# Performance work log

Hardware: AMD Instinct MI355X
Metric: run time of the kernel (lower is better)

The kernel has to match this reference:

```python
import jax, jax.numpy as jnp
import numpy as np

B, L, D = 2, 2048, 2048
HQ, HKV = 32, 8
HD = D // HQ            # 64
G = HQ // HKV           # 4


def setup_inputs() -> dict:
    key = jax.random.key(0)
    ks = jax.random.split(key, 9)
    s = 1.0 / np.sqrt(D)
    return {
        "x": jax.random.normal(ks[0], (B, L, D), jnp.float32),
        "Wq": jax.random.normal(ks[1], (D, HQ * HD), jnp.float32) * s,
        "bq": jnp.zeros((HQ * HD,), jnp.float32),
        "Wk": jax.random.normal(ks[2], (D, HKV * HD), jnp.float32) * s,
        "bk": jnp.zeros((HKV * HD,), jnp.float32),
        "Wv": jax.random.normal(ks[3], (D, HKV * HD), jnp.float32) * s,
        "bv": jnp.zeros((HKV * HD,), jnp.float32),
        "Wo": jax.random.normal(ks[4], (HQ * HD, D), jnp.float32) * s,
        "bo": jnp.zeros((D,), jnp.float32),
    }


def reference(x, Wq, bq, Wk, bk, Wv, bv, Wo, bo):
    # projections
    q = x @ Wq + bq                                   # [B, L, HQ*HD]
    k = x @ Wk + bk                                   # [B, L, HKV*HD]
    v = x @ Wv + bv
    # split heads; group q heads by kv head: [B, HKV, G, L, HD]
    q = q.reshape(B, L, HKV, G, HD).transpose(0, 2, 3, 1, 4)
    k = k.reshape(B, L, HKV, HD).transpose(0, 2, 1, 3)   # [B, HKV, L, HD]
    v = v.reshape(B, L, HKV, HD).transpose(0, 2, 1, 3)
    scale = 1.0 / np.sqrt(HD)
    # scores [B, HKV, G, Lq, Lk] -- same math as repeat_kv + matmul
    scores = jnp.einsum('bhgqd,bhkd->bhgqk', q, k) * scale
    attn = jax.nn.softmax(scores, axis=-1)
    ctx = jnp.einsum('bhgqk,bhkd->bhgqd', attn, v)       # [B, HKV, G, L, HD]
    # merge heads back to [B, L, HQ*HD]
    ctx = ctx.transpose(0, 3, 1, 2, 4).reshape(B, L, HQ * HD)
    return ctx @ Wo + bo
```

## Files before the change

kernel.cpp:

```cpp
#include <hip/hip_runtime.h>
#include <cstdint>
#include <cstring>


#define L_SEQ 2048
#define D_MODEL 2048
#define M_ROWS 4096
#define KV_COLS 512
#define ATTN_SCALE 0.18033688011112042f

typedef __bf16 bf16x8 __attribute__((ext_vector_type(8)));
typedef float f32x4 __attribute__((ext_vector_type(4)));
typedef float f32x16 __attribute__((ext_vector_type(16)));

__device__ __forceinline__ f32x4 zero4() {
    f32x4 v; v[0] = 0.f; v[1] = 0.f; v[2] = 0.f; v[3] = 0.f; return v;
}

__device__ __forceinline__ unsigned short f2bf(float x) {
    unsigned u = __builtin_bit_cast(unsigned, x);
    u = (u + 0x7FFFu + ((u >> 16) & 1u)) >> 16;
    return (unsigned short)u;
}

__device__ __forceinline__ unsigned pk_bf16(float a, float b) {
#if __has_builtin(__builtin_amdgcn_cvt_pk_bf16_f32)
    typedef __bf16 bf16x2 __attribute__((ext_vector_type(2)));
    bf16x2 r = __builtin_amdgcn_cvt_pk_bf16_f32(a, b);
    return __builtin_bit_cast(unsigned, r);
#else
    return (unsigned)f2bf(a) | ((unsigned)f2bf(b) << 16);
#endif
}

__device__ __forceinline__ f32x4 mfma16(uint4 a, uint4 b, f32x4 c) {
    return __builtin_amdgcn_mfma_f32_16x16x32_bf16(
        __builtin_bit_cast(bf16x8, a), __builtin_bit_cast(bf16x8, b), c, 0, 0, 0);
}
__device__ __forceinline__ f32x16 mfma32(uint4 a, uint4 b, f32x16 c) {
    return __builtin_amdgcn_mfma_f32_32x32x16_bf16(
        __builtin_bit_cast(bf16x8, a), __builtin_bit_cast(bf16x8, b), c, 0, 0, 0);
}

__device__ __forceinline__ void gl_lds16(const unsigned short* g, unsigned short* l) {
    __builtin_amdgcn_global_load_lds(
        (const __attribute__((address_space(1))) unsigned int*)g,
        (__attribute__((address_space(3))) unsigned int*)l, 16, 0, 0);
}

#if __has_builtin(__builtin_amdgcn_exp2f)
#define EXP2F(x) __builtin_amdgcn_exp2f(x)
#else
#define EXP2F(x) exp2f(x)
#endif

__device__ __forceinline__ void permswap32(unsigned& a, unsigned& b) {
    asm("v_permlane32_swap_b32 %0, %1" : "+v"(a), "+v"(b));
}


__global__ __launch_bounds__(256) void cast_x_kernel(const float* __restrict__ in,
                                                     unsigned short* __restrict__ out,
                                                     int n4) {
    int i = blockIdx.x * 256 + threadIdx.x;
    if (i >= n4) return;
    float4 v = ((const float4*)in)[i];
    uint2 o;
    o.x = pk_bf16(v.x, v.y);
    o.y = pk_bf16(v.z, v.w);
    ((uint2*)out)[i] = o;
}

__global__ __launch_bounds__(256) void transpose_cast_kernel(const float* __restrict__ in,
                                                             unsigned short* __restrict__ out,
                                                             int N, int row_off) {
    __shared__ float tile[32][33];
    const int n0 = blockIdx.x * 32, k0 = blockIdx.y * 32;
    const int tc = threadIdx.x & 31, tr = threadIdx.x >> 5;
#pragma unroll
    for (int i = 0; i < 4; ++i)
        tile[tr + i * 8][tc] = in[(size_t)(k0 + tr + i * 8) * N + n0 + tc];
    __syncthreads();
#pragma unroll
    for (int i = 0; i < 4; ++i)
        out[(size_t)(row_off + n0 + tr + i * 8) * 2048 + k0 + tc] = f2bf(tile[tc][tr + i * 8]);
}

__global__ __launch_bounds__(256) void transpose_v_kernel(const unsigned short* __restrict__ Vb,
                                                          unsigned short* __restrict__ Vt) {
    __shared__ unsigned short tile[32][33];
    const int c0 = blockIdx.x * 32, l0 = blockIdx.y * 32, b = blockIdx.z;
    const int tc = threadIdx.x & 31, tr = threadIdx.x >> 5;
#pragma unroll
    for (int i = 0; i < 4; ++i)
        tile[tr + i * 8][tc] = Vb[(size_t)(b * 2048 + l0 + tr + i * 8) * KV_COLS + c0 + tc];
    __syncthreads();
#pragma unroll
    for (int i = 0; i < 4; ++i)
        Vt[(size_t)(b * 512 + c0 + tr + i * 8) * 2048 + l0 + tc] = tile[tc][tr + i * 8];
}


__device__ __forceinline__ void gemm_core_2048(const unsigned short* __restrict__ A,
                                               const unsigned short* __restrict__ Bt,
                                               int m_block, int n_block,
                                               unsigned short* smA, unsigned short* smB,
                                               f32x4 acc[4][4]) {
    const int tid = threadIdx.x;
    const int w = tid >> 6, lane = tid & 63;
    const int wm = w >> 1, wn = w & 1;
    const int lr = lane & 15, lg = lane >> 4;

#pragma unroll
    for (int i = 0; i < 4; ++i)
#pragma unroll
        for (int j = 0; j < 4; ++j) acc[i][j] = zero4();

    const int rowA = m_block * 128 + w * 32 + (lane >> 2);
    const int rowB = n_block * 128 + w * 32 + (lane >> 2);
    const int kcol = (lane & 3) * 8;
    const unsigned short* gA0 = A + (size_t)rowA * 2048 + kcol;
    const unsigned short* gA1 = gA0 + (size_t)16 * 2048;
    const unsigned short* gB0 = Bt + (size_t)rowB * 2048 + kcol;
    const unsigned short* gB1 = gB0 + (size_t)16 * 2048;
    unsigned short* lA0 = smA + (w * 32) * 32;
    unsigned short* lA1 = smA + (w * 32 + 16) * 32;
    unsigned short* lB0 = smB + (w * 32) * 32;
    unsigned short* lB1 = smB + (w * 32 + 16) * 32;

    for (int kt = 0; kt < 64; ++kt) {
        gl_lds16(gA0 + kt * 32, lA0);
        gl_lds16(gA1 + kt * 32, lA1);
        gl_lds16(gB0 + kt * 32, lB0);
        gl_lds16(gB1 + kt * 32, lB1);
        __syncthreads();
        uint4 af[4], bfg[4];
#pragma unroll
        for (int i = 0; i < 4; ++i)
            af[i] = *(const uint4*)(smA + (wm * 64 + i * 16 + lr) * 32 + lg * 8);
#pragma unroll
        for (int j = 0; j < 4; ++j)
            bfg[j] = *(const uint4*)(smB + (wn * 64 + j * 16 + lr) * 32 + lg * 8);
#pragma unroll
        for (int i = 0; i < 4; ++i)
#pragma unroll
            for (int j = 0; j < 4; ++j)
                acc[i][j] = mfma16(af[i], bfg[j], acc[i][j]);
        __syncthreads();
    }
}

__global__ __launch_bounds__(256) void gemm_qkv_kernel(
    const unsigned short* __restrict__ Xb, const unsigned short* __restrict__ Wt,
    const float* __restrict__ bq, const float* __restrict__ bk, const float* __restrict__ bv,
    unsigned short* __restrict__ Qb, unsigned short* __restrict__ Kb,
    unsigned short* __restrict__ Vb) {
    __shared__ __align__(16) unsigned short smA[128 * 32];
    __shared__ __align__(16) unsigned short smB[128 * 32];
    f32x4 acc[4][4];
    gemm_core_2048(Xb, Wt, blockIdx.x, blockIdx.y, smA, smB, acc);

    const int tid = threadIdx.x;
    const int w = tid >> 6, lane = tid & 63;
    const int wm = w >> 1, wn = w & 1;
    const int lr = lane & 15, lg = lane >> 4;
    const int nbase = blockIdx.y * 128;

    unsigned short* outp; int ldo, noff; const float* bias; float scale;
    if (nbase < 2048)      { outp = Qb; ldo = 2048; noff = 0;    bias = bq; scale = 1.f; }
    else if (nbase < 2560) { outp = Kb; ldo = 512;  noff = 2048; bias = bk; scale = ATTN_SCALE; }
    else                   { outp = Vb; ldo = 512;  noff = 2560; bias = bv; scale = 1.f; }

#pragma unroll
    for (int i = 0; i < 4; ++i) {
        const int mrow = blockIdx.x * 128 + wm * 64 + i * 16 + lg * 4;
#pragma unroll
        for (int j = 0; j < 4; ++j) {
            const int nloc = nbase + wn * 64 + j * 16 + lr - noff;
            const float bb = bias[nloc];
#pragma unroll
            for (int r = 0; r < 4; ++r)
                outp[(size_t)(mrow + r) * ldo + nloc] = f2bf((acc[i][j][r] + bb) * scale);
        }
    }
}

__global__ __launch_bounds__(256) void gemm_out_kernel(
    const unsigned short* __restrict__ Cb, const unsigned short* __restrict__ Wot,
    const float* __restrict__ bo, float* __restrict__ out) {
    __shared__ __align__(16) unsigned short smA[128 * 32];
    __shared__ __align__(16) unsigned short smB[128 * 32];
    f32x4 acc[4][4];
    gemm_core_2048(Cb, Wot, blockIdx.x, blockIdx.y, smA, smB, acc);

    const int tid = threadIdx.x;
    const int w = tid >> 6, lane = tid & 63;
    const int wm = w >> 1, wn = w & 1;
    const int lr = lane & 15, lg = lane >> 4;

#pragma unroll
    for (int i = 0; i < 4; ++i) {
        const int mrow = blockIdx.x * 128 + wm * 64 + i * 16 + lg * 4;
#pragma unroll
        for (int j = 0; j < 4; ++j) {
            const int ncol = blockIdx.y * 128 + wn * 64 + j * 16 + lr;
            const float bb = bo[ncol];
#pragma unroll
            for (int r = 0; r < 4; ++r)
                out[(size_t)(mrow + r) * 2048 + ncol] = acc[i][j][r] + bb;
        }
    }
}


__global__ __launch_bounds__(512, 2) void attn_kernel(const unsigned short* __restrict__ Qb,
                                                      const unsigned short* __restrict__ Kb,
                                                      const unsigned short* __restrict__ Vtg,
                                                      unsigned short* __restrict__ ctx) {
    __shared__ __align__(16) unsigned short smem[32768];

    const int qt = blockIdx.x, hq = blockIdx.y, b = blockIdx.z;
    const int kvh = hq >> 2;
    const int tid = threadIdx.x;
    const int w = tid >> 6, lane = tid & 63;
    const int l31 = lane & 31, h = lane >> 5;

    const int qbase = qt * 512 + w * 64;
    uint4 qf[2][4];
#pragma unroll
    for (int u = 0; u < 2; ++u) {
        const unsigned short* qp =
            Qb + (size_t)(b * L_SEQ + qbase + u * 32 + l31) * 2048 + hq * 64;
#pragma unroll
        for (int dh = 0; dh < 4; ++dh)
            qf[u][dh] = *(const uint4*)(qp + dh * 16 + h * 8);
    }

    f32x16 o00, o01, o10, o11;
#pragma unroll
    for (int r = 0; r < 16; ++r) { o00[r] = 0.f; o01[r] = 0.f; o10[r] = 0.f; o11[r] = 0.f; }
    float l_acc0 = 0.f, l_acc1 = 0.f;

    const size_t kbase = (size_t)(b * L_SEQ) * KV_COLS + kvh * 64;
    const size_t vbase = (size_t)((b * 8 + kvh) * 64) * 2048;

    const int rrk = lane >> 3, cpk = lane & 7;
    const int drv = lane >> 4, cpv = lane & 15;

    unsigned short* ksC = smem;
    unsigned short* vtC = smem + 8192;
    unsigned short* ksN = smem + 16384;
    unsigned short* vtN = smem + 24576;

    auto stage = [&](int T, unsigned short* KS, unsigned short* VT) {
        const int k0s = T * 128;
#pragma unroll
        for (int s = 0; s < 2; ++s) {
            const int blk = w * 2 + s;
            gl_lds16(Kb + kbase + (size_t)(k0s + blk * 8 + rrk) * KV_COLS + ((cpk ^ rrk) * 8),
                     KS + blk * 512);
            const int d = blk * 4 + drv;
            gl_lds16(Vtg + vbase + (size_t)d * 2048 + k0s + ((cpv ^ (d & 15)) * 8),
                     VT + blk * 512);
        }
    };

    stage(0, ksC, vtC);
    __syncthreads();

    for (int t = 0; t < 16; ++t) {
        if (t < 15) stage(t + 1, ksN, vtN);

#pragma unroll
        for (int c = 0; c < 4; ++c) {
            uint4 kf[4];
#pragma unroll
            for (int dh = 0; dh < 4; ++dh)
                kf[dh] = *(const uint4*)&ksC[(c * 32 + l31) * 64 +
                                             (((dh * 2 + h) ^ (l31 & 7)) * 8)];
            unsigned E0[4][2], E1[4][2];
#pragma unroll
            for (int u = 0; u < 2; ++u) {
                f32x16 s;
#pragma unroll
                for (int r = 0; r < 16; ++r) s[r] = 0.f;
                __builtin_amdgcn_s_setprio(1);
#pragma unroll
                for (int dh = 0; dh < 4; ++dh) s = mfma32(kf[dh], qf[u][dh], s);
                __builtin_amdgcn_s_setprio(0);
                float lsum = 0.f;
#pragma unroll
                for (int g = 0; g < 4; ++g) {
                    float e0 = EXP2F(s[4 * g + 0]);
                    float e1 = EXP2F(s[4 * g + 1]);
                    float e2 = EXP2F(s[4 * g + 2]);
                    float e3 = EXP2F(s[4 * g + 3]);
                    lsum += (e0 + e1) + (e2 + e3);
                    if (u == 0) { E0[g][0] = pk_bf16(e0, e1); E0[g][1] = pk_bf16(e2, e3); }
                    else        { E1[g][0] = pk_bf16(e0, e1); E1[g][1] = pk_bf16(e2, e3); }
                }
                if (u == 0) l_acc0 += lsum; else l_acc1 += lsum;
            }
#pragma unroll
            for (int tau = 0; tau < 2; ++tau) {
                const int pos = ((c * 4 + tau * 2 + h) ^ (l31 & 15)) * 8;
                uint4 vf0 = *(const uint4*)&vtC[(size_t)l31 * 128 + pos];
                uint4 vf1 = *(const uint4*)&vtC[(size_t)(32 + l31) * 128 + pos];
                {
                    unsigned x0 = E0[2 * tau][0], z0 = E0[2 * tau + 1][0];
                    unsigned x1 = E0[2 * tau][1], z1 = E0[2 * tau + 1][1];
                    permswap32(x0, z0);
                    permswap32(x1, z1);
                    uint4 pf; pf.x = x0; pf.y = x1; pf.z = z0; pf.w = z1;
                    __builtin_amdgcn_s_setprio(1);
                    o00 = mfma32(vf0, pf, o00);
                    o01 = mfma32(vf1, pf, o01);
                    __builtin_amdgcn_s_setprio(0);
                }
                {
                    unsigned x0 = E1[2 * tau][0], z0 = E1[2 * tau + 1][0];
                    unsigned x1 = E1[2 * tau][1], z1 = E1[2 * tau + 1][1];
                    permswap32(x0, z0);
                    permswap32(x1, z1);
                    uint4 pf; pf.x = x0; pf.y = x1; pf.z = z0; pf.w = z1;
                    __builtin_amdgcn_s_setprio(1);
                    o10 = mfma32(vf0, pf, o10);
                    o11 = mfma32(vf1, pf, o11);
                    __builtin_amdgcn_s_setprio(0);
                }
            }
        }

        __syncthreads();
        unsigned short* tk = ksC; ksC = ksN; ksN = tk;
        unsigned short* tv = vtC; vtC = vtN; vtN = tv;
    }

    unsigned* ep = (unsigned*)smem + w * 1088;
#pragma unroll
    for (int u = 0; u < 2; ++u) {
        const float la = u ? l_acc1 : l_acc0;
        const float l_tot = la + __shfl_xor(la, 32, 64);
        const float rl = 1.f / l_tot;
#pragma unroll
        for (int dt = 0; dt < 2; ++dt) {
            const f32x16& o = u ? (dt ? o11 : o10) : (dt ? o01 : o00);
#pragma unroll
            for (int g = 0; g < 4; ++g)
#pragma unroll
                for (int p = 0; p < 2; ++p) {
                    const int dv = dt * 16 + 4 * g + 2 * h + p;
                    ep[l31 * 34 + dv] =
                        pk_bf16(o[4 * g + 2 * p] * rl, o[4 * g + 2 * p + 1] * rl);
                }
        }
        __builtin_amdgcn_s_waitcnt(0);
#pragma unroll
        for (int p = 0; p < 4; ++p) {
            const int qr = (lane >> 3) + p * 8;
            const int cch = lane & 7;
            uint4 vv = *(const uint4*)((const unsigned short*)ep + qr * 68 + cch * 8);
            *(uint4*)(ctx + (size_t)(b * L_SEQ + qbase + u * 32 + qr) * 2048 +
                      hq * 64 + cch * 8) = vv;
        }
        __builtin_amdgcn_s_waitcnt(0);
    }
}


extern "C" void kernel_launch(void* const* d_in, const int* in_sizes, int n_in,
                              void* d_out, int out_size, void* d_ws, size_t ws_size,
                              hipStream_t stream) {
    const float* x  = (const float*)d_in[0];
    const float* Wq = (const float*)d_in[1];
    const float* bq = (const float*)d_in[2];
    const float* Wk = (const float*)d_in[3];
    const float* bk = (const float*)d_in[4];
    const float* Wv = (const float*)d_in[5];
    const float* bv = (const float*)d_in[6];
    const float* Wo = (const float*)d_in[7];
    const float* bo = (const float*)d_in[8];
    float* out = (float*)d_out;

    char* ws = (char*)d_ws;
    size_t off = 0;
    auto alloc = [&](size_t bytes) {
        char* p = ws + off;
        off += (bytes + 255) & ~(size_t)255;
        return p;
    };
    unsigned short* Wqkvt = (unsigned short*)alloc((size_t)3072 * 2048 * 2);
    unsigned short* Wot   = (unsigned short*)alloc((size_t)2048 * 2048 * 2);
    unsigned short* Xb    = (unsigned short*)alloc((size_t)M_ROWS * 2048 * 2);
    unsigned short* Qb    = (unsigned short*)alloc((size_t)M_ROWS * 2048 * 2);
    unsigned short* Kb    = (unsigned short*)alloc((size_t)M_ROWS * KV_COLS * 2);
    unsigned short* Vb    = (unsigned short*)alloc((size_t)M_ROWS * KV_COLS * 2);
    unsigned short* Vt    = (unsigned short*)alloc((size_t)M_ROWS * KV_COLS * 2);
    unsigned short* Cb    = Xb;

    cast_x_kernel<<<(M_ROWS * 2048 / 4 + 255) / 256, 256, 0, stream>>>(x, Xb,
                                                                       M_ROWS * 2048 / 4);
    transpose_cast_kernel<<<dim3(64, 64), 256, 0, stream>>>(Wq, Wqkvt, 2048, 0);
    transpose_cast_kernel<<<dim3(16, 64), 256, 0, stream>>>(Wk, Wqkvt, 512, 2048);
    transpose_cast_kernel<<<dim3(16, 64), 256, 0, stream>>>(Wv, Wqkvt, 512, 2560);
    transpose_cast_kernel<<<dim3(64, 64), 256, 0, stream>>>(Wo, Wot, 2048, 0);
    gemm_qkv_kernel<<<dim3(32, 24), 256, 0, stream>>>(Xb, Wqkvt, bq, bk, bv, Qb, Kb, Vb);
    transpose_v_kernel<<<dim3(16, 64, 2), 256, 0, stream>>>(Vb, Vt);
    attn_kernel<<<dim3(4, 32, 2), 512, 0, stream>>>(Qb, Kb, Vt, Cb);
    gemm_out_kernel<<<dim3(32, 16), 256, 0, stream>>>(Cb, Wot, bo, out);
}
```

Before: 319.0 us.

## Triple-buffer attention K/V tiles with vmcnt barriers and remap blocks to XCDs

The attention kernel now keeps three LDS buffers instead of two and prefetches K/V tiles two iterations ahead. Per-iteration __syncthreads is replaced by an s_waitcnt vmcnt(N) plus s_barrier, so later loads can stay in flight. The 3D grid becomes a 1D grid of 256 blocks with a swizzle that places the four query tiles of a head (same KV) on the same XCD for L2 reuse. LDS use per block grows from 64KB to 96KB, which may cut occupancy below the two blocks per CU requested by the launch bounds.

```diff
diff --git a/kernel.cpp b/kernel.cpp
--- a/kernel.cpp
+++ b/kernel.cpp
@@ -56,6 +56,19 @@
 
 __device__ __forceinline__ void permswap32(unsigned& a, unsigned& b) {
     asm("v_permlane32_swap_b32 %0, %1" : "+v"(a), "+v"(b));
+}
+
+__device__ __forceinline__ void bar_vm(int keep ) {
+}
+__device__ __forceinline__ void bar_vm4() {
+    asm volatile("s_waitcnt vmcnt(4)" ::: "memory");
+    __builtin_amdgcn_s_barrier();
+    asm volatile("" ::: "memory");
+}
+__device__ __forceinline__ void bar_vm0() {
+    asm volatile("s_waitcnt vmcnt(0)" ::: "memory");
+    __builtin_amdgcn_s_barrier();
+    asm volatile("" ::: "memory");
 }
 
 
@@ -217,10 +230,15 @@
                                                       const unsigned short* __restrict__ Kb,
                                                       const unsigned short* __restrict__ Vtg,
                                                       unsigned short* __restrict__ ctx) {
-    __shared__ __align__(16) unsigned short smem[32768];
-
-    const int qt = blockIdx.x, hq = blockIdx.y, b = blockIdx.z;
+    __shared__ __align__(16) unsigned short smem[49152];
+
+    const int p = blockIdx.x;
+    const int x = p & 7, j = p >> 3;
+    const int group = x * 8 + (j >> 2);
+    const int qt = j & 3;
+    const int hq = group & 31, b = group >> 5;
     const int kvh = hq >> 2;
+
     const int tid = threadIdx.x;
     const int w = tid >> 6, lane = tid & 63;
     const int l31 = lane & 31, h = lane >> 5;
@@ -247,12 +265,13 @@
     const int rrk = lane >> 3, cpk = lane & 7;
     const int drv = lane >> 4, cpv = lane & 15;
 
-    unsigned short* ksC = smem;
-    unsigned short* vtC = smem + 8192;
-    unsigned short* ksN = smem + 16384;
-    unsigned short* vtN = smem + 24576;
-
-    auto stage = [&](int T, unsigned short* KS, unsigned short* VT) {
+    unsigned short* bC  = smem;
+    unsigned short* bN  = smem + 16384;
+    unsigned short* bNN = smem + 32768;
+
+    auto stage = [&](int T, unsigned short* SL) {
+        unsigned short* KS = SL;
+        unsigned short* VT = SL + 8192;
         const int k0s = T * 128;
 #pragma unroll
         for (int s = 0; s < 2; ++s) {
@@ -265,11 +284,15 @@
         }
     };
 
-    stage(0, ksC, vtC);
-    __syncthreads();
+    stage(0, bC);
+    stage(1, bN);
+    bar_vm4();
 
     for (int t = 0; t < 16; ++t) {
-        if (t < 15) stage(t + 1, ksN, vtN);
+        if (t <= 13) stage(t + 2, bNN);
+
+        unsigned short* ksC = bC;
+        unsigned short* vtC = bC + 8192;
 
 #pragma unroll
         for (int c = 0; c < 4; ++c) {
@@ -331,11 +354,14 @@
             }
         }
 
-        __syncthreads();
-        unsigned short* tk = ksC; ksC = ksN; ksN = tk;
-        unsigned short* tv = vtC; vtC = vtN; vtN = tv;
-    }
-
+        if (t <= 13)      bar_vm4();
+        else if (t == 14) bar_vm0();
+        else              { __builtin_amdgcn_s_barrier(); asm volatile("" ::: "memory"); }
+
+        unsigned short* tmp = bC; bC = bN; bN = bNN; bNN = tmp;
+    }
+
+    __syncthreads();
     unsigned* ep = (unsigned*)smem + w * 1088;
 #pragma unroll
     for (int u = 0; u < 2; ++u) {
@@ -348,16 +374,16 @@
 #pragma unroll
             for (int g = 0; g < 4; ++g)
 #pragma unroll
-                for (int p = 0; p < 2; ++p) {
-                    const int dv = dt * 16 + 4 * g + 2 * h + p;
+                for (int pq = 0; pq < 2; ++pq) {
+                    const int dv = dt * 16 + 4 * g + 2 * h + pq;
                     ep[l31 * 34 + dv] =
-                        pk_bf16(o[4 * g + 2 * p] * rl, o[4 * g + 2 * p + 1] * rl);
+                        pk_bf16(o[4 * g + 2 * pq] * rl, o[4 * g + 2 * pq + 1] * rl);
                 }
         }
         __builtin_amdgcn_s_waitcnt(0);
 #pragma unroll
-        for (int p = 0; p < 4; ++p) {
-            const int qr = (lane >> 3) + p * 8;
+        for (int pq = 0; pq < 4; ++pq) {
+            const int qr = (lane >> 3) + pq * 8;
             const int cch = lane & 7;
             uint4 vv = *(const uint4*)((const unsigned short*)ep + qr * 68 + cch * 8);
             *(uint4*)(ctx + (size_t)(b * L_SEQ + qbase + u * 32 + qr) * 2048 +
@@ -406,6 +432,6 @@
     transpose_cast_kernel<<<dim3(64, 64), 256, 0, stream>>>(Wo, Wot, 2048, 0);
     gemm_qkv_kernel<<<dim3(32, 24), 256, 0, stream>>>(Xb, Wqkvt, bq, bk, bv, Qb, Kb, Vb);
     transpose_v_kernel<<<dim3(16, 64, 2), 256, 0, stream>>>(Vb, Vt);
-    attn_kernel<<<dim3(4, 32, 2), 512, 0, stream>>>(Qb, Kb, Vt, Cb);
+    attn_kernel<<<dim3(256), 512, 0, stream>>>(Qb, Kb, Vt, Cb);
     gemm_out_kernel<<<dim3(32, 16), 256, 0, stream>>>(Cb, Wot, bo, out);
 }
```

Measured after the change: 342.8 us. 1.07x slower.

## Rewrite projection GEMMs with larger tiles, double-buffered swizzled LDS, and staged epilogue

Applied to the files above, without the earlier changes.

Both projection GEMMs move to 512-thread blocks with larger output tiles (256x256 for QKV, 128x256 for the output projection) and a 64-wide K step. Loads go into double-buffered LDS with an XOR swizzle, so the next tile is fetched while MFMAs run on the current one and the extra barrier per iteration is gone. MFMA sections are wrapped in setprio. The QKV epilogue stages results through LDS to emit 16-byte bf16 stores. Risks include lower occupancy (one block per CU, large LDS) and fewer blocks than CUs for the QKV grid (192 blocks), which can leave CUs idle.

```diff
diff --git a/kernel.cpp b/kernel.cpp
--- a/kernel.cpp
+++ b/kernel.cpp
@@ -101,113 +101,241 @@
 }
 
 
-__device__ __forceinline__ void gemm_core_2048(const unsigned short* __restrict__ A,
-                                               const unsigned short* __restrict__ Bt,
-                                               int m_block, int n_block,
-                                               unsigned short* smA, unsigned short* smB,
-                                               f32x4 acc[4][4]) {
-    const int tid = threadIdx.x;
-    const int w = tid >> 6, lane = tid & 63;
-    const int wm = w >> 1, wn = w & 1;
-    const int lr = lane & 15, lg = lane >> 4;
-
-#pragma unroll
-    for (int i = 0; i < 4; ++i)
-#pragma unroll
-        for (int j = 0; j < 4; ++j) acc[i][j] = zero4();
-
-    const int rowA = m_block * 128 + w * 32 + (lane >> 2);
-    const int rowB = n_block * 128 + w * 32 + (lane >> 2);
-    const int kcol = (lane & 3) * 8;
-    const unsigned short* gA0 = A + (size_t)rowA * 2048 + kcol;
-    const unsigned short* gA1 = gA0 + (size_t)16 * 2048;
-    const unsigned short* gB0 = Bt + (size_t)rowB * 2048 + kcol;
-    const unsigned short* gB1 = gB0 + (size_t)16 * 2048;
-    unsigned short* lA0 = smA + (w * 32) * 32;
-    unsigned short* lA1 = smA + (w * 32 + 16) * 32;
-    unsigned short* lB0 = smB + (w * 32) * 32;
-    unsigned short* lB1 = smB + (w * 32 + 16) * 32;
-
-    for (int kt = 0; kt < 64; ++kt) {
-        gl_lds16(gA0 + kt * 32, lA0);
-        gl_lds16(gA1 + kt * 32, lA1);
-        gl_lds16(gB0 + kt * 32, lB0);
-        gl_lds16(gB1 + kt * 32, lB1);
-        __syncthreads();
-        uint4 af[4], bfg[4];
-#pragma unroll
-        for (int i = 0; i < 4; ++i)
-            af[i] = *(const uint4*)(smA + (wm * 64 + i * 16 + lr) * 32 + lg * 8);
-#pragma unroll
-        for (int j = 0; j < 4; ++j)
-            bfg[j] = *(const uint4*)(smB + (wn * 64 + j * 16 + lr) * 32 + lg * 8);
-#pragma unroll
-        for (int i = 0; i < 4; ++i)
-#pragma unroll
-            for (int j = 0; j < 4; ++j)
-                acc[i][j] = mfma16(af[i], bfg[j], acc[i][j]);
-        __syncthreads();
-    }
-}
-
-__global__ __launch_bounds__(256) void gemm_qkv_kernel(
+__global__ __launch_bounds__(512, 1) void gemm_qkv_kernel(
     const unsigned short* __restrict__ Xb, const unsigned short* __restrict__ Wt,
     const float* __restrict__ bq, const float* __restrict__ bk, const float* __restrict__ bv,
     unsigned short* __restrict__ Qb, unsigned short* __restrict__ Kb,
     unsigned short* __restrict__ Vb) {
-    __shared__ __align__(16) unsigned short smA[128 * 32];
-    __shared__ __align__(16) unsigned short smB[128 * 32];
-    f32x4 acc[4][4];
-    gemm_core_2048(Xb, Wt, blockIdx.x, blockIdx.y, smA, smB, acc);
-
+    __shared__ __align__(16) char smem[131072];
+
+    const int mb = blockIdx.x, nb = blockIdx.y;
     const int tid = threadIdx.x;
     const int w = tid >> 6, lane = tid & 63;
-    const int wm = w >> 1, wn = w & 1;
+    const int wm = w >> 2, wn = w & 3;
     const int lr = lane & 15, lg = lane >> 4;
-    const int nbase = blockIdx.y * 128;
-
+    const int rr = lane >> 3, cp = lane & 7;
+
+    f32x4 acc[8][4];
+#pragma unroll
+    for (int i = 0; i < 8; ++i)
+#pragma unroll
+        for (int j = 0; j < 4; ++j) acc[i][j] = zero4();
+
+    const size_t arow0 = (size_t)mb * 256;
+    const size_t brow0 = (size_t)nb * 256;
+
+    auto stage = [&](int kt, int d) {
+        const int k8 = kt * 64 + ((cp ^ rr) * 8);
+#pragma unroll
+        for (int s = 0; s < 4; ++s) {
+            const int c = w * 4 + s;
+            gl_lds16(Xb + (arow0 + c * 8 + rr) * 2048 + k8,
+                     (unsigned short*)(smem + d * 65536 + c * 1024));
+            gl_lds16(Wt + (brow0 + c * 8 + rr) * 2048 + k8,
+                     (unsigned short*)(smem + d * 65536 + 32768 + c * 1024));
+        }
+    };
+
+    stage(0, 0);
+    __syncthreads();
+
+    for (int t = 0; t < 32; ++t) {
+        const int d = t & 1;
+        if (t < 31) stage(t + 1, d ^ 1);
+
+        const char* Ab = smem + d * 65536;
+        const char* Bb = smem + d * 65536 + 32768;
+        auto rdA = [&](int mi, int k) -> uint4 {
+            const int row = wm * 128 + mi * 16 + lr;
+            return *(const uint4*)(Ab + row * 128 + (((k * 4 + lg) ^ (lr & 7)) * 16));
+        };
+        auto rdB = [&](int nj, int k) -> uint4 {
+            const int row = wn * 64 + nj * 16 + lr;
+            return *(const uint4*)(Bb + row * 128 + (((k * 4 + lg) ^ (lr & 7)) * 16));
+        };
+
+        uint4 fa[4][2], fb[2][2];
+#pragma unroll
+        for (int mi = 0; mi < 4; ++mi) { fa[mi][0] = rdA(mi, 0); fa[mi][1] = rdA(mi, 1); }
+#pragma unroll
+        for (int nj = 0; nj < 2; ++nj) { fb[nj][0] = rdB(nj, 0); fb[nj][1] = rdB(nj, 1); }
+        __builtin_amdgcn_s_setprio(1);
+#pragma unroll
+        for (int mi = 0; mi < 4; ++mi)
+#pragma unroll
+            for (int nj = 0; nj < 2; ++nj) {
+                acc[mi][nj] = mfma16(fa[mi][0], fb[nj][0], acc[mi][nj]);
+                acc[mi][nj] = mfma16(fa[mi][1], fb[nj][1], acc[mi][nj]);
+            }
+        __builtin_amdgcn_s_setprio(0);
+#pragma unroll
+        for (int nj = 0; nj < 2; ++nj) { fb[nj][0] = rdB(nj + 2, 0); fb[nj][1] = rdB(nj + 2, 1); }
+        __builtin_amdgcn_s_setprio(1);
+#pragma unroll
+        for (int mi = 0; mi < 4; ++mi)
+#pragma unroll
+            for (int nj = 0; nj < 2; ++nj) {
+                acc[mi][nj + 2] = mfma16(fa[mi][0], fb[nj][0], acc[mi][nj + 2]);
+                acc[mi][nj + 2] = mfma16(fa[mi][1], fb[nj][1], acc[mi][nj + 2]);
+            }
+        __builtin_amdgcn_s_setprio(0);
+#pragma unroll
+        for (int mi = 0; mi < 4; ++mi) { fa[mi][0] = rdA(mi + 4, 0); fa[mi][1] = rdA(mi + 4, 1); }
+        __builtin_amdgcn_s_setprio(1);
+#pragma unroll
+        for (int mi = 0; mi < 4; ++mi)
+#pragma unroll
+            for (int nj = 0; nj < 2; ++nj) {
+                acc[mi + 4][nj + 2] = mfma16(fa[mi][0], fb[nj][0], acc[mi + 4][nj + 2]);
+                acc[mi + 4][nj + 2] = mfma16(fa[mi][1], fb[nj][1], acc[mi + 4][nj + 2]);
+            }
+        __builtin_amdgcn_s_setprio(0);
+#pragma unroll
+        for (int nj = 0; nj < 2; ++nj) { fb[nj][0] = rdB(nj, 0); fb[nj][1] = rdB(nj, 1); }
+        __builtin_amdgcn_s_setprio(1);
+#pragma unroll
+        for (int mi = 0; mi < 4; ++mi)
+#pragma unroll
+            for (int nj = 0; nj < 2; ++nj) {
+                acc[mi + 4][nj] = mfma16(fa[mi][0], fb[nj][0], acc[mi + 4][nj]);
+                acc[mi + 4][nj] = mfma16(fa[mi][1], fb[nj][1], acc[mi + 4][nj]);
+            }
+        __builtin_amdgcn_s_setprio(0);
+
+        __syncthreads();
+    }
+
+    const int nbase = nb * 256;
     unsigned short* outp; int ldo, noff; const float* bias; float scale;
     if (nbase < 2048)      { outp = Qb; ldo = 2048; noff = 0;    bias = bq; scale = 1.f; }
     else if (nbase < 2560) { outp = Kb; ldo = 512;  noff = 2048; bias = bk; scale = ATTN_SCALE; }
     else                   { outp = Vb; ldo = 512;  noff = 2560; bias = bv; scale = 1.f; }
 
-#pragma unroll
-    for (int i = 0; i < 4; ++i) {
-        const int mrow = blockIdx.x * 128 + wm * 64 + i * 16 + lg * 4;
-#pragma unroll
-        for (int j = 0; j < 4; ++j) {
-            const int nloc = nbase + wn * 64 + j * 16 + lr - noff;
-            const float bb = bias[nloc];
-#pragma unroll
-            for (int r = 0; r < 4; ++r)
-                outp[(size_t)(mrow + r) * ldo + nloc] = f2bf((acc[i][j][r] + bb) * scale);
-        }
-    }
-}
-
-__global__ __launch_bounds__(256) void gemm_out_kernel(
+    float* ep = (float*)(smem + w * 16384);
+#pragma unroll
+    for (int pair = 0; pair < 2; ++pair) {
+#pragma unroll
+        for (int mi = 0; mi < 8; ++mi)
+#pragma unroll
+            for (int jj = 0; jj < 2; ++jj)
+#pragma unroll
+                for (int r = 0; r < 4; ++r)
+                    ep[(mi * 16 + lg * 4 + r) * 32 + jj * 16 + lr] = acc[mi][pair * 2 + jj][r];
+        __builtin_amdgcn_s_waitcnt(0);
+#pragma unroll
+        for (int p = 0; p < 8; ++p) {
+            const int row = p * 16 + (lane >> 2);
+            const int q = lane & 3;
+            const float* v = ep + row * 32 + q * 8;
+            const int ncol = nbase + wn * 64 + pair * 32 + q * 8 - noff;
+            const float4 b0 = *(const float4*)(bias + ncol);
+            const float4 b1 = *(const float4*)(bias + ncol + 4);
+            uint4 o;
+            o.x = pk_bf16((v[0] + b0.x) * scale, (v[1] + b0.y) * scale);
+            o.y = pk_bf16((v[2] + b0.z) * scale, (v[3] + b0.w) * scale);
+            o.z = pk_bf16((v[4] + b1.x) * scale, (v[5] + b1.y) * scale);
+            o.w = pk_bf16((v[6] + b1.z) * scale, (v[7] + b1.w) * scale);
+            *(uint4*)(outp + (size_t)(mb * 256 + wm * 128 + row) * ldo + ncol) = o;
+        }
+        __builtin_amdgcn_s_waitcnt(0);
+    }
+}
+
+
+__global__ __launch_bounds__(512, 1) void gemm_out_kernel(
     const unsigned short* __restrict__ Cb, const unsigned short* __restrict__ Wot,
     const float* __restrict__ bo, float* __restrict__ out) {
-    __shared__ __align__(16) unsigned short smA[128 * 32];
-    __shared__ __align__(16) unsigned short smB[128 * 32];
-    f32x4 acc[4][4];
-    gemm_core_2048(Cb, Wot, blockIdx.x, blockIdx.y, smA, smB, acc);
-
+    __shared__ __align__(16) char smem[98304];
+
+    const int mb = blockIdx.x, nb = blockIdx.y;
     const int tid = threadIdx.x;
     const int w = tid >> 6, lane = tid & 63;
-    const int wm = w >> 1, wn = w & 1;
+    const int wm = w >> 2, wn = w & 3;
     const int lr = lane & 15, lg = lane >> 4;
-
-#pragma unroll
-    for (int i = 0; i < 4; ++i) {
-        const int mrow = blockIdx.x * 128 + wm * 64 + i * 16 + lg * 4;
-#pragma unroll
-        for (int j = 0; j < 4; ++j) {
-            const int ncol = blockIdx.y * 128 + wn * 64 + j * 16 + lr;
+    const int rr = lane >> 3, cp = lane & 7;
+
+    f32x4 acc[4][4];
+#pragma unroll
+    for (int i = 0; i < 4; ++i)
+#pragma unroll
+        for (int j = 0; j < 4; ++j) acc[i][j] = zero4();
+
+    const size_t arow0 = (size_t)mb * 128;
+    const size_t brow0 = (size_t)nb * 256;
+
+    auto stage = [&](int kt, int d) {
+        const int k8 = kt * 64 + ((cp ^ rr) * 8);
+#pragma unroll
+        for (int s = 0; s < 2; ++s) {
+            const int c = w * 2 + s;
+            gl_lds16(Cb + (arow0 + c * 8 + rr) * 2048 + k8,
+                     (unsigned short*)(smem + d * 49152 + c * 1024));
+        }
+#pragma unroll
+        for (int s = 0; s < 4; ++s) {
+            const int c = w * 4 + s;
+            gl_lds16(Wot + (brow0 + c * 8 + rr) * 2048 + k8,
+                     (unsigned short*)(smem + d * 49152 + 16384 + c * 1024));
+        }
+    };
+
+    stage(0, 0);
+    __syncthreads();
+
+    for (int t = 0; t < 32; ++t) {
+        const int d = t & 1;
+        if (t < 31) stage(t + 1, d ^ 1);
+
+        const char* Ab = smem + d * 49152;
+        const char* Bb = smem + d * 49152 + 16384;
+        auto rdA = [&](int mi, int k) -> uint4 {
+            const int row = wm * 64 + mi * 16 + lr;
+            return *(const uint4*)(Ab + row * 128 + (((k * 4 + lg) ^ (lr & 7)) * 16));
+        };
+        auto rdB = [&](int nj, int k) -> uint4 {
+            const int row = wn * 64 + nj * 16 + lr;
+            return *(const uint4*)(Bb + row * 128 + (((k * 4 + lg) ^ (lr & 7)) * 16));
+        };
+
+        uint4 fa[4][2], fb[2][2];
+#pragma unroll
+        for (int mi = 0; mi < 4; ++mi) { fa[mi][0] = rdA(mi, 0); fa[mi][1] = rdA(mi, 1); }
+#pragma unroll
+        for (int nj = 0; nj < 2; ++nj) { fb[nj][0] = rdB(nj, 0); fb[nj][1] = rdB(nj, 1); }
+        __builtin_amdgcn_s_setprio(1);
+#pragma unroll
+        for (int mi = 0; mi < 4; ++mi)
+#pragma unroll
+            for (int nj = 0; nj < 2; ++nj) {
+                acc[mi][nj] = mfma16(fa[mi][0], fb[nj][0], acc[mi][nj]);
+                acc[mi][nj] = mfma16(fa[mi][1], fb[nj][1], acc[mi][nj]);
+            }
+        __builtin_amdgcn_s_setprio(0);
+#pragma unroll
+        for (int nj = 0; nj < 2; ++nj) { fb[nj][0] = rdB(nj + 2, 0); fb[nj][1] = rdB(nj + 2, 1); }
+        __builtin_amdgcn_s_setprio(1);
+#pragma unroll
+        for (int mi = 0; mi < 4; ++mi)
+#pragma unroll
+            for (int nj = 0; nj < 2; ++nj) {
+                acc[mi][nj + 2] = mfma16(fa[mi][0], fb[nj][0], acc[mi][nj + 2]);
+                acc[mi][nj + 2] = mfma16(fa[mi][1], fb[nj][1], acc[mi][nj + 2]);
+            }
+        __builtin_amdgcn_s_setprio(0);
+
+        __syncthreads();
+    }
+
+#pragma unroll
+    for (int mi = 0; mi < 4; ++mi) {
+        const int mrow = mb * 128 + wm * 64 + mi * 16 + lg * 4;
+#pragma unroll
+        for (int nj = 0; nj < 4; ++nj) {
+            const int ncol = nb * 256 + wn * 64 + nj * 16 + lr;
             const float bb = bo[ncol];
 #pragma unroll
             for (int r = 0; r < 4; ++r)
-                out[(size_t)(mrow + r) * 2048 + ncol] = acc[i][j][r] + bb;
+                out[(size_t)(mrow + r) * 2048 + ncol] = acc[mi][nj][r] + bb;
         }
     }
 }
@@ -404,8 +532,8 @@
     transpose_cast_kernel<<<dim3(16, 64), 256, 0, stream>>>(Wk, Wqkvt, 512, 2048);
     transpose_cast_kernel<<<dim3(16, 64), 256, 0, stream>>>(Wv, Wqkvt, 512, 2560);
     transpose_cast_kernel<<<dim3(64, 64), 256, 0, stream>>>(Wo, Wot, 2048, 0);
-    gemm_qkv_kernel<<<dim3(32, 24), 256, 0, stream>>>(Xb, Wqkvt, bq, bk, bv, Qb, Kb, Vb);
+    gemm_qkv_kernel<<<dim3(16, 12), 512, 0, stream>>>(Xb, Wqkvt, bq, bk, bv, Qb, Kb, Vb);
     transpose_v_kernel<<<dim3(16, 64, 2), 256, 0, stream>>>(Vb, Vt);
     attn_kernel<<<dim3(4, 32, 2), 512, 0, stream>>>(Qb, Kb, Vt, Cb);
-    gemm_out_kernel<<<dim3(32, 16), 256, 0, stream>>>(Cb, Wot, bo, out);
-}
+    gemm_out_kernel<<<dim3(32, 8), 512, 0, stream>>>(Cb, Wot, bo, out);
+}
```

After: 325.5 us. 2.0% more time.

## Rewrite projection GEMMs with triple-buffered LDS ring, swizzle, and 8 waves

Applied to the files above, without the earlier changes.

Replaces the single-buffered GEMM core used by the QKV and output projections. The new core uses a 3-slot LDS ring with K-tile 64, XOR-swizzled LDS layout and vmcnt-based waits, so global loads overlap MFMA work. Blocks grow to 512 threads (8 waves, each computing 64x32), and the QKV epilogue is staged through LDS to write 16-byte bf16 vectors. This costs about 96KB of LDS per block, which limits occupancy to one block per CU, and adds a dependency on exact vmcnt counting.

```diff
diff --git a/kernel.cpp b/kernel.cpp
--- a/kernel.cpp
+++ b/kernel.cpp
@@ -101,113 +101,152 @@
 }
 
 
-__device__ __forceinline__ void gemm_core_2048(const unsigned short* __restrict__ A,
+__device__ __forceinline__ void gemm_ring_core(const unsigned short* __restrict__ A,
                                                const unsigned short* __restrict__ Bt,
-                                               int m_block, int n_block,
-                                               unsigned short* smA, unsigned short* smB,
-                                               f32x4 acc[4][4]) {
+                                               int arow0, int brow0,
+                                               char* smem, f32x4 acc[4][2]) {
     const int tid = threadIdx.x;
     const int w = tid >> 6, lane = tid & 63;
-    const int wm = w >> 1, wn = w & 1;
+    const int wm = w >> 2, wn = w & 3;
     const int lr = lane & 15, lg = lane >> 4;
+    const int rr = lane >> 3, cp = lane & 7;
 
 #pragma unroll
     for (int i = 0; i < 4; ++i)
 #pragma unroll
-        for (int j = 0; j < 4; ++j) acc[i][j] = zero4();
-
-    const int rowA = m_block * 128 + w * 32 + (lane >> 2);
-    const int rowB = n_block * 128 + w * 32 + (lane >> 2);
-    const int kcol = (lane & 3) * 8;
-    const unsigned short* gA0 = A + (size_t)rowA * 2048 + kcol;
-    const unsigned short* gA1 = gA0 + (size_t)16 * 2048;
-    const unsigned short* gB0 = Bt + (size_t)rowB * 2048 + kcol;
-    const unsigned short* gB1 = gB0 + (size_t)16 * 2048;
-    unsigned short* lA0 = smA + (w * 32) * 32;
-    unsigned short* lA1 = smA + (w * 32 + 16) * 32;
-    unsigned short* lB0 = smB + (w * 32) * 32;
-    unsigned short* lB1 = smB + (w * 32 + 16) * 32;
-
-    for (int kt = 0; kt < 64; ++kt) {
-        gl_lds16(gA0 + kt * 32, lA0);
-        gl_lds16(gA1 + kt * 32, lA1);
-        gl_lds16(gB0 + kt * 32, lB0);
-        gl_lds16(gB1 + kt * 32, lB1);
-        __syncthreads();
-        uint4 af[4], bfg[4];
-#pragma unroll
-        for (int i = 0; i < 4; ++i)
-            af[i] = *(const uint4*)(smA + (wm * 64 + i * 16 + lr) * 32 + lg * 8);
-#pragma unroll
-        for (int j = 0; j < 4; ++j)
-            bfg[j] = *(const uint4*)(smB + (wn * 64 + j * 16 + lr) * 32 + lg * 8);
-#pragma unroll
-        for (int i = 0; i < 4; ++i)
-#pragma unroll
-            for (int j = 0; j < 4; ++j)
-                acc[i][j] = mfma16(af[i], bfg[j], acc[i][j]);
-        __syncthreads();
-    }
-}
-
-__global__ __launch_bounds__(256) void gemm_qkv_kernel(
+        for (int j = 0; j < 2; ++j) acc[i][j] = zero4();
+
+    auto stage = [&](int kt, int slot) {
+        char* base = smem + slot * 32768;
+        const int k8 = kt * 64 + ((cp ^ rr) * 8);
+#pragma unroll
+        for (int s = 0; s < 2; ++s) {
+            const int c = w * 2 + s;
+            gl_lds16(A + (size_t)(arow0 + c * 8 + rr) * 2048 + k8,
+                     (unsigned short*)(base + c * 1024));
+            gl_lds16(Bt + (size_t)(brow0 + c * 8 + rr) * 2048 + k8,
+                     (unsigned short*)(base + 16384 + c * 1024));
+        }
+    };
+
+    stage(0, 0);
+    stage(1, 1);
+
+    for (int t = 0; t < 32; ++t) {
+        if (t < 31) asm volatile("s_waitcnt vmcnt(4)" ::: "memory");
+        else        asm volatile("s_waitcnt vmcnt(0)" ::: "memory");
+        __builtin_amdgcn_s_barrier();
+        asm volatile("" ::: "memory");
+
+        if (t <= 29) stage(t + 2, (t + 2) % 3);
+
+        const char* Ab = smem + (t % 3) * 32768;
+        const char* Bb = Ab + 16384;
+
+        uint4 fa[4][2], fb[2][2];
+#pragma unroll
+        for (int mi = 0; mi < 4; ++mi) {
+            const int row = wm * 64 + mi * 16 + lr;
+#pragma unroll
+            for (int ks = 0; ks < 2; ++ks)
+                fa[mi][ks] = *(const uint4*)(Ab + row * 128 +
+                                             (((ks * 4 + lg) ^ (lr & 7)) * 16));
+        }
+#pragma unroll
+        for (int nj = 0; nj < 2; ++nj) {
+            const int row = wn * 32 + nj * 16 + lr;
+#pragma unroll
+            for (int ks = 0; ks < 2; ++ks)
+                fb[nj][ks] = *(const uint4*)(Bb + row * 128 +
+                                             (((ks * 4 + lg) ^ (lr & 7)) * 16));
+        }
+        __builtin_amdgcn_s_setprio(1);
+#pragma unroll
+        for (int mi = 0; mi < 4; ++mi)
+#pragma unroll
+            for (int nj = 0; nj < 2; ++nj) {
+                acc[mi][nj] = mfma16(fa[mi][0], fb[nj][0], acc[mi][nj]);
+                acc[mi][nj] = mfma16(fa[mi][1], fb[nj][1], acc[mi][nj]);
+            }
+        __builtin_amdgcn_s_setprio(0);
+    }
+}
+
+__global__ __launch_bounds__(512, 1) void gemm_qkv_kernel(
     const unsigned short* __restrict__ Xb, const unsigned short* __restrict__ Wt,
     const float* __restrict__ bq, const float* __restrict__ bk, const float* __restrict__ bv,
     unsigned short* __restrict__ Qb, unsigned short* __restrict__ Kb,
     unsigned short* __restrict__ Vb) {
-    __shared__ __align__(16) unsigned short smA[128 * 32];
-    __shared__ __align__(16) unsigned short smB[128 * 32];
-    f32x4 acc[4][4];
-    gemm_core_2048(Xb, Wt, blockIdx.x, blockIdx.y, smA, smB, acc);
+    __shared__ __align__(16) char smem[98304];
+
+    const int mb = blockIdx.x, nb = blockIdx.y;
+    f32x4 acc[4][2];
+    gemm_ring_core(Xb, Wt, mb * 128, nb * 128, smem, acc);
 
     const int tid = threadIdx.x;
     const int w = tid >> 6, lane = tid & 63;
-    const int wm = w >> 1, wn = w & 1;
+    const int wm = w >> 2, wn = w & 3;
     const int lr = lane & 15, lg = lane >> 4;
-    const int nbase = blockIdx.y * 128;
-
+
+    const int nbase = nb * 128;
     unsigned short* outp; int ldo, noff; const float* bias; float scale;
     if (nbase < 2048)      { outp = Qb; ldo = 2048; noff = 0;    bias = bq; scale = 1.f; }
     else if (nbase < 2560) { outp = Kb; ldo = 512;  noff = 2048; bias = bk; scale = ATTN_SCALE; }
     else                   { outp = Vb; ldo = 512;  noff = 2560; bias = bv; scale = 1.f; }
 
-#pragma unroll
-    for (int i = 0; i < 4; ++i) {
-        const int mrow = blockIdx.x * 128 + wm * 64 + i * 16 + lg * 4;
-#pragma unroll
-        for (int j = 0; j < 4; ++j) {
-            const int nloc = nbase + wn * 64 + j * 16 + lr - noff;
-            const float bb = bias[nloc];
+    __syncthreads();
+    float* ep = (float*)(smem + (size_t)w * 8192);
+#pragma unroll
+    for (int mi = 0; mi < 4; ++mi)
+#pragma unroll
+        for (int nj = 0; nj < 2; ++nj)
 #pragma unroll
             for (int r = 0; r < 4; ++r)
-                outp[(size_t)(mrow + r) * ldo + nloc] = f2bf((acc[i][j][r] + bb) * scale);
-        }
-    }
-}
-
-__global__ __launch_bounds__(256) void gemm_out_kernel(
+                ep[(mi * 16 + lg * 4 + r) * 32 + nj * 16 + lr] = acc[mi][nj][r];
+    __builtin_amdgcn_s_waitcnt(0);
+#pragma unroll
+    for (int p = 0; p < 4; ++p) {
+        const int row = p * 16 + (lane >> 2);
+        const int cc = lane & 3;
+        const float* v = ep + row * 32 + cc * 8;
+        const float4 va = *(const float4*)v;
+        const float4 vb2 = *(const float4*)(v + 4);
+        const int nloc = nbase + wn * 32 + cc * 8 - noff;
+        const float4 b0 = *(const float4*)(bias + nloc);
+        const float4 b1 = *(const float4*)(bias + nloc + 4);
+        uint4 o;
+        o.x = pk_bf16((va.x + b0.x) * scale, (va.y + b0.y) * scale);
+        o.y = pk_bf16((va.z + b0.z) * scale, (va.w + b0.w) * scale);
+        o.z = pk_bf16((vb2.x + b1.x) * scale, (vb2.y + b1.y) * scale);
+        o.w = pk_bf16((vb2.z + b1.z) * scale, (vb2.w + b1.w) * scale);
+        *(uint4*)(outp + (size_t)(mb * 128 + wm * 64 + row) * ldo + nloc) = o;
+    }
+}
+
+__global__ __launch_bounds__(512, 1) void gemm_out_kernel(
     const unsigned short* __restrict__ Cb, const unsigned short* __restrict__ Wot,
     const float* __restrict__ bo, float* __restrict__ out) {
-    __shared__ __align__(16) unsigned short smA[128 * 32];
-    __shared__ __align__(16) unsigned short smB[128 * 32];
-    f32x4 acc[4][4];
-    gemm_core_2048(Cb, Wot, blockIdx.x, blockIdx.y, smA, smB, acc);
+    __shared__ __align__(16) char smem[98304];
+
+    const int mb = blockIdx.x, nb = blockIdx.y;
+    f32x4 acc[4][2];
+    gemm_ring_core(Cb, Wot, mb * 128, nb * 128, smem, acc);
 
     const int tid = threadIdx.x;
     const int w = tid >> 6, lane = tid & 63;
-    const int wm = w >> 1, wn = w & 1;
+    const int wm = w >> 2, wn = w & 3;
     const int lr = lane & 15, lg = lane >> 4;
 
 #pragma unroll
-    for (int i = 0; i < 4; ++i) {
-        const int mrow = blockIdx.x * 128 + wm * 64 + i * 16 + lg * 4;
-#pragma unroll
-        for (int j = 0; j < 4; ++j) {
-            const int ncol = blockIdx.y * 128 + wn * 64 + j * 16 + lr;
+    for (int mi = 0; mi < 4; ++mi) {
+        const int mrow = mb * 128 + wm * 64 + mi * 16 + lg * 4;
+#pragma unroll
+        for (int nj = 0; nj < 2; ++nj) {
+            const int ncol = nb * 128 + wn * 32 + nj * 16 + lr;
             const float bb = bo[ncol];
 #pragma unroll
             for (int r = 0; r < 4; ++r)
-                out[(size_t)(mrow + r) * 2048 + ncol] = acc[i][j][r] + bb;
+                out[(size_t)(mrow + r) * 2048 + ncol] = acc[mi][nj][r] + bb;
         }
     }
 }
@@ -404,8 +443,8 @@
     transpose_cast_kernel<<<dim3(16, 64), 256, 0, stream>>>(Wk, Wqkvt, 512, 2048);
     transpose_cast_kernel<<<dim3(16, 64), 256, 0, stream>>>(Wv, Wqkvt, 512, 2560);
     transpose_cast_kernel<<<dim3(64, 64), 256, 0, stream>>>(Wo, Wot, 2048, 0);
-    gemm_qkv_kernel<<<dim3(32, 24), 256, 0, stream>>>(Xb, Wqkvt, bq, bk, bv, Qb, Kb, Vb);
+    gemm_qkv_kernel<<<dim3(32, 24), 512, 0, stream>>>(Xb, Wqkvt, bq, bk, bv, Qb, Kb, Vb);
     transpose_v_kernel<<<dim3(16, 64, 2), 256, 0, stream>>>(Vb, Vt);
     attn_kernel<<<dim3(4, 32, 2), 512, 0, stream>>>(Qb, Kb, Vt, Cb);
-    gemm_out_kernel<<<dim3(32, 16), 256, 0, stream>>>(Cb, Wot, bo, out);
-}
+    gemm_out_kernel<<<dim3(32, 16), 512, 0, stream>>>(Cb, Wot, bo, out);
+}
```

After: 310.5 us. 1.03x faster.
